# Performance work log

Measured on AMD Instinct MI355X. Metric: run time of the kernel, lower is better.

The kernel has to match this reference:

```python
import jax, jax.numpy as jnp
import numpy as np

DT = 0.001
TAU_MEM = 0.01
TAU_SYN = 0.005
THRESHOLD = 1.0
INITIAL_STATE = 0.0
SS_BETA = 100.0  # SuperSpike surrogate slope (Zenke & Ganguli)


@jax.custom_vjp
def superspike(x):
    # Heaviside spike in forward
    return (x > 0).astype(x.dtype)

def _ss_fwd(x):
    return superspike(x), x

def _ss_bwd(x, g):
    # fast-sigmoid surrogate gradient
    return (g / (SS_BETA * jnp.abs(x) + 1.0) ** 2,)

superspike.defvjp(_ss_fwd, _ss_bwd)


def setup_inputs() -> dict:
    key = jax.random.key(0)
    k1, k2 = jax.random.split(key)
    B, T, IN, OUT = 64, 1024, 256, 256
    inputs = jax.random.normal(k1, (B, T, IN), dtype=jnp.float32)
    w = jax.random.normal(k2, (IN, OUT), dtype=jnp.float32) * 4.0  # scale=4.0 in __init__
    return {"inputs": inputs, "w": w}


def _simulate_mem(inputs, w):
    # inputs: [B, T, IN], w: [IN, OUT]
    x = jnp.matmul(inputs, w)  # [B, T, OUT]
    T = x.shape[1]
    dcy_mem = jnp.exp(jnp.asarray(-DT / (TAU_MEM + 1e-16), dtype=x.dtype))
    scl_mem = 1.0 - dcy_mem
    dcy_syn = jnp.exp(jnp.asarray(-DT / (TAU_SYN + 1e-16), dtype=x.dtype))

    zeros0 = jnp.zeros_like(x[:, 0])  # initial_state = 0

    def step(carry, x_t):
        syn, mem = carry
        new_syn = dcy_syn * syn + x_t
        new_mem = dcy_mem * mem + scl_mem * syn  # uses OLD syn
        out = superspike(mem - THRESHOLD)        # spike from OLD mem
        new_mem = new_mem * (1.0 - out)          # reset
        return (new_syn, new_mem), new_mem

    # loop runs over t = 0 .. T-2 (matches `for t in range(nb_steps - 1)`)
    xs = jnp.swapaxes(x[:, : T - 1], 0, 1)  # [T-1, B, OUT]
    _, mems = jax.lax.scan(step, (zeros0, zeros0), xs)
    mems = jnp.swapaxes(mems, 0, 1)  # [B, T-1, OUT]
    # prepend the initial stored state (zeros, since initial_state=0)
    U = jnp.concatenate([zeros0[:, None, :], mems], axis=1)  # [B, T, OUT]
    return U


def reference(inputs, w):
    # monitor == 'mem' -> return membrane potential trace U
    return _simulate_mem(inputs, w)
```

## Files before the change

kernel.cpp:

```cpp
#include <hip/hip_runtime.h>
#include <cmath>

typedef short bf16x8 __attribute__((ext_vector_type(8)));
typedef float f32x4 __attribute__((ext_vector_type(4)));
typedef unsigned short us4 __attribute__((ext_vector_type(4)));

#define T_DIM 1024
#define LDA 72

__device__ __forceinline__ unsigned short rtn_bf16(float f) {
    unsigned u = __float_as_uint(f);
    return (unsigned short)((u + 0x7FFFu + ((u >> 16) & 1u)) >> 16);
}
__device__ __forceinline__ float bf_to_f(unsigned short h) {
    return __uint_as_float(((unsigned)h) << 16);
}

__global__ __launch_bounds__(256) void lif_wsplit(const float* __restrict__ w,
                                                  unsigned short* __restrict__ wT1,
                                                  unsigned short* __restrict__ wT2,
                                                  unsigned short* __restrict__ wT3) {
    const int id = blockIdx.x * 256 + threadIdx.x;
    const int k = id >> 8, n = id & 255;
    const float f = w[id];
    const unsigned short h1 = rtn_bf16(f);
    const float r1 = f - bf_to_f(h1);
    const unsigned short h2 = rtn_bf16(r1);
    const float r2 = r1 - bf_to_f(h2);
    const unsigned short h3 = rtn_bf16(r2);
    const int o = n * 256 + k;
    wT1[o] = h1; wT2[o] = h2; wT3[o] = h3;
}

__global__ __launch_bounds__(256) void lif_gemm_mfma(const float* __restrict__ in,
                                                     const unsigned short* __restrict__ wT1,
                                                     const unsigned short* __restrict__ wT2,
                                                     const unsigned short* __restrict__ wT3,
                                                     float* __restrict__ xbuf) {
    __shared__ unsigned short As[3][128 * LDA];

    const int tid  = threadIdx.x;
    const int bm   = blockIdx.x;
    const int bn   = blockIdx.y;
    const int wave = tid >> 6;
    const int lane = tid & 63;
    const int l15  = lane & 15;
    const int quad = lane >> 4;
    const int wm   = (wave >> 1) * 64;
    const int wn   = (wave & 1) * 64;

    f32x4 acc[4][4];
    #pragma unroll
    for (int i = 0; i < 4; ++i)
        #pragma unroll
        for (int j = 0; j < 4; ++j) acc[i][j] = (f32x4){0.f, 0.f, 0.f, 0.f};

    const int r  = tid >> 1;
    const int hf = tid & 1;
    const float* arow = in + (size_t)(bm * 128 + r) * 256;

    for (int kt = 0; kt < 4; ++kt) {
        const int k0 = kt * 64;
        float4 av[8];
        #pragma unroll
        for (int j = 0; j < 8; ++j)
            av[j] = *(const float4*)(arow + k0 + (hf * 8 + j) * 4);

        __syncthreads();
        #pragma unroll
        for (int j = 0; j < 8; ++j) {
            const int kl = (hf * 8 + j) * 4;
            float fv[4] = {av[j].x, av[j].y, av[j].z, av[j].w};
            us4 o1, o2, o3;
            #pragma unroll
            for (int i = 0; i < 4; ++i) {
                const unsigned short h1 = rtn_bf16(fv[i]);
                const float r1 = fv[i] - bf_to_f(h1);
                const unsigned short h2 = rtn_bf16(r1);
                const float r2 = r1 - bf_to_f(h2);
                const unsigned short h3 = rtn_bf16(r2);
                o1[i] = h1; o2[i] = h2; o3[i] = h3;
            }
            *(us4*)&As[0][r * LDA + kl] = o1;
            *(us4*)&As[1][r * LDA + kl] = o2;
            *(us4*)&As[2][r * LDA + kl] = o3;
        }
        __syncthreads();

        #pragma unroll
        for (int ks = 0; ks < 2; ++ks) {
            bf16x8 af[3][4];
            #pragma unroll
            for (int mt = 0; mt < 4; ++mt) {
                const int row = wm + mt * 16 + l15;
                const int ko  = ks * 32 + quad * 8;
                af[0][mt] = *(const bf16x8*)&As[0][row * LDA + ko];
                af[1][mt] = *(const bf16x8*)&As[1][row * LDA + ko];
                af[2][mt] = *(const bf16x8*)&As[2][row * LDA + ko];
            }
            #pragma unroll
            for (int nt = 0; nt < 4; ++nt) {
                const int ncol = bn * 128 + wn + nt * 16 + l15;
                const size_t wo = (size_t)ncol * 256 + k0 + ks * 32 + quad * 8;
                const bf16x8 b1 = *(const bf16x8*)(wT1 + wo);
                const bf16x8 b2 = *(const bf16x8*)(wT2 + wo);
                const bf16x8 b3 = *(const bf16x8*)(wT3 + wo);
                #pragma unroll
                for (int mt = 0; mt < 4; ++mt) {
                    f32x4 a = acc[mt][nt];
                    a = __builtin_amdgcn_mfma_f32_16x16x32_bf16(af[0][mt], b1, a, 0, 0, 0);
                    a = __builtin_amdgcn_mfma_f32_16x16x32_bf16(af[0][mt], b2, a, 0, 0, 0);
                    a = __builtin_amdgcn_mfma_f32_16x16x32_bf16(af[1][mt], b1, a, 0, 0, 0);
                    a = __builtin_amdgcn_mfma_f32_16x16x32_bf16(af[1][mt], b2, a, 0, 0, 0);
                    a = __builtin_amdgcn_mfma_f32_16x16x32_bf16(af[0][mt], b3, a, 0, 0, 0);
                    a = __builtin_amdgcn_mfma_f32_16x16x32_bf16(af[2][mt], b1, a, 0, 0, 0);
                    acc[mt][nt] = a;
                }
            }
        }
    }

    #pragma unroll
    for (int mt = 0; mt < 4; ++mt) {
        #pragma unroll
        for (int nt = 0; nt < 4; ++nt) {
            const int C = bn * 128 + wn + nt * 16 + l15;
            const int Rb = bm * 128 + wm + mt * 16 + quad * 4;
            #pragma unroll
            for (int reg = 0; reg < 4; ++reg)
                xbuf[(size_t)(Rb + reg) * 256 + C] = acc[mt][nt][reg];
        }
    }
}

__global__ __launch_bounds__(64) void lif_scan(const float* __restrict__ xbuf,
                                               float* __restrict__ U,
                                               double dcy_syn, double dcy_mem,
                                               double scl_mem) {
    const int b = blockIdx.x >> 2;
    const int o = (blockIdx.x & 3) * 64 + threadIdx.x;

    double syn = 0.0, mem = 0.0;
    U[(size_t)b * T_DIM * 256 + o] = 0.0f;

    const float* xp = xbuf + (size_t)b * T_DIM * 256 + o;
    float* up = U + (size_t)b * T_DIM * 256 + o;

    int tl = 0;
    for (; tl + 32 <= T_DIM - 1; tl += 32) {
        float xr[32];
        #pragma unroll
        for (int j = 0; j < 32; ++j) xr[j] = xp[(size_t)(tl + j) * 256];
        #pragma unroll
        for (int j = 0; j < 32; ++j) {
            double nm = dcy_mem * mem + scl_mem * syn;
            if (mem - 1.0 > 0.0) nm = 0.0;
            syn = dcy_syn * syn + (double)xr[j];
            mem = nm;
            up[(size_t)(tl + j + 1) * 256] = (float)mem;
        }
    }
    for (; tl < T_DIM - 1; ++tl) {
        const double x = (double)xp[(size_t)tl * 256];
        double nm = dcy_mem * mem + scl_mem * syn;
        if (mem - 1.0 > 0.0) nm = 0.0;
        syn = dcy_syn * syn + x;
        mem = nm;
        up[(size_t)(tl + 1) * 256] = (float)mem;
    }
}

extern "C" void kernel_launch(void* const* d_in, const int* in_sizes, int n_in,
                              void* d_out, int out_size, void* d_ws, size_t ws_size,
                              hipStream_t stream) {
    const float* in = (const float*)d_in[0];
    const float* w  = (const float*)d_in[1];
    float* U = (float*)d_out;

    const double dcy_mem = exp(-0.001 / (0.01  + 1e-16));
    const double dcy_syn = exp(-0.001 / (0.005 + 1e-16));
    const double scl_mem = 1.0 - dcy_mem;

    char* ws = (char*)d_ws;
    unsigned short* wT1 = (unsigned short*)ws;
    unsigned short* wT2 = (unsigned short*)(ws + 131072);
    unsigned short* wT3 = (unsigned short*)(ws + 262144);
    float* xbuf = (float*)(ws + 524288);

    lif_wsplit<<<dim3(256), dim3(256), 0, stream>>>(w, wT1, wT2, wT3);
    lif_gemm_mfma<<<dim3(512, 2), dim3(256), 0, stream>>>(in, wT1, wT2, wT3, xbuf);
    lif_scan<<<dim3(256), dim3(64), 0, stream>>>(xbuf, U, dcy_syn, dcy_mem, scl_mem);
}
```

Before: 206.4 us.

## Swizzle GEMM LDS tiles, truncate-split bf16, and stage scan inputs via LDS

The GEMM A-tile now uses an XOR-swizzled 64-wide LDS layout with 8-element vector stores instead of padded rows. The first two bf16 split terms use truncation rather than round-to-nearest. The scan kernel prefetches 64-timestep chunks of x as float4 loads into registers, then into shared memory, double-buffering the next chunk while computing. This targets the scan's strided scalar global loads and LDS bank conflicts, at the cost of extra syncs and register pressure.

```diff
diff --git a/kernel.cpp b/kernel.cpp
--- a/kernel.cpp
+++ b/kernel.cpp
@@ -3,10 +3,9 @@
 
 typedef short bf16x8 __attribute__((ext_vector_type(8)));
 typedef float f32x4 __attribute__((ext_vector_type(4)));
-typedef unsigned short us4 __attribute__((ext_vector_type(4)));
+typedef unsigned short us8v __attribute__((ext_vector_type(8)));
 
 #define T_DIM 1024
-#define LDA 72
 
 __device__ __forceinline__ unsigned short rtn_bf16(float f) {
     unsigned u = __float_as_uint(f);
@@ -14,6 +13,17 @@
 }
 __device__ __forceinline__ float bf_to_f(unsigned short h) {
     return __uint_as_float(((unsigned)h) << 16);
+}
+
+__device__ __forceinline__ void split3(float f, unsigned short& h1,
+                                       unsigned short& h2, unsigned short& h3) {
+    unsigned u = __float_as_uint(f);
+    h1 = (unsigned short)(u >> 16);
+    float r1 = f - __uint_as_float(u & 0xFFFF0000u);
+    unsigned u1 = __float_as_uint(r1);
+    h2 = (unsigned short)(u1 >> 16);
+    float r2 = r1 - __uint_as_float(u1 & 0xFFFF0000u);
+    h3 = rtn_bf16(r2);
 }
 
 __global__ __launch_bounds__(256) void lif_wsplit(const float* __restrict__ w,
@@ -22,12 +32,8 @@
                                                   unsigned short* __restrict__ wT3) {
     const int id = blockIdx.x * 256 + threadIdx.x;
     const int k = id >> 8, n = id & 255;
-    const float f = w[id];
-    const unsigned short h1 = rtn_bf16(f);
-    const float r1 = f - bf_to_f(h1);
-    const unsigned short h2 = rtn_bf16(r1);
-    const float r2 = r1 - bf_to_f(h2);
-    const unsigned short h3 = rtn_bf16(r2);
+    unsigned short h1, h2, h3;
+    split3(w[id], h1, h2, h3);
     const int o = n * 256 + k;
     wT1[o] = h1; wT2[o] = h2; wT3[o] = h3;
 }
@@ -37,7 +43,7 @@
                                                      const unsigned short* __restrict__ wT2,
                                                      const unsigned short* __restrict__ wT3,
                                                      float* __restrict__ xbuf) {
-    __shared__ unsigned short As[3][128 * LDA];
+    __shared__ unsigned short As[3][128 * 64];
 
     const int tid  = threadIdx.x;
     const int bm   = blockIdx.x;
@@ -57,46 +63,45 @@
 
     const int r  = tid >> 1;
     const int hf = tid & 1;
-    const float* arow = in + (size_t)(bm * 128 + r) * 256;
+    const int rx = r & 7;
+    const float* arow = in + (size_t)(bm * 128 + r) * 256 + hf * 32;
 
     for (int kt = 0; kt < 4; ++kt) {
         const int k0 = kt * 64;
         float4 av[8];
         #pragma unroll
         for (int j = 0; j < 8; ++j)
-            av[j] = *(const float4*)(arow + k0 + (hf * 8 + j) * 4);
-
-        __syncthreads();
-        #pragma unroll
-        for (int j = 0; j < 8; ++j) {
-            const int kl = (hf * 8 + j) * 4;
-            float fv[4] = {av[j].x, av[j].y, av[j].z, av[j].w};
-            us4 o1, o2, o3;
-            #pragma unroll
-            for (int i = 0; i < 4; ++i) {
-                const unsigned short h1 = rtn_bf16(fv[i]);
-                const float r1 = fv[i] - bf_to_f(h1);
-                const unsigned short h2 = rtn_bf16(r1);
-                const float r2 = r1 - bf_to_f(h2);
-                const unsigned short h3 = rtn_bf16(r2);
+            av[j] = *(const float4*)(arow + k0 + j * 4);
+
+        __syncthreads();
+        #pragma unroll
+        for (int j2 = 0; j2 < 4; ++j2) {
+            const float fv[8] = {av[2*j2].x, av[2*j2].y, av[2*j2].z, av[2*j2].w,
+                                 av[2*j2+1].x, av[2*j2+1].y, av[2*j2+1].z, av[2*j2+1].w};
+            us8v o1, o2, o3;
+            #pragma unroll
+            for (int i = 0; i < 8; ++i) {
+                unsigned short h1, h2, h3;
+                split3(fv[i], h1, h2, h3);
                 o1[i] = h1; o2[i] = h2; o3[i] = h3;
             }
-            *(us4*)&As[0][r * LDA + kl] = o1;
-            *(us4*)&As[1][r * LDA + kl] = o2;
-            *(us4*)&As[2][r * LDA + kl] = o3;
+            const int cp = ((hf * 4 + j2) ^ rx) * 8;
+            *(us8v*)&As[0][r * 64 + cp] = o1;
+            *(us8v*)&As[1][r * 64 + cp] = o2;
+            *(us8v*)&As[2][r * 64 + cp] = o3;
         }
         __syncthreads();
 
         #pragma unroll
         for (int ks = 0; ks < 2; ++ks) {
             bf16x8 af[3][4];
+            const int ko = ((ks * 4 + quad) ^ (l15 & 7)) * 8;
             #pragma unroll
             for (int mt = 0; mt < 4; ++mt) {
-                const int row = wm + mt * 16 + l15;
-                const int ko  = ks * 32 + quad * 8;
-                af[0][mt] = *(const bf16x8*)&As[0][row * LDA + ko];
-                af[1][mt] = *(const bf16x8*)&As[1][row * LDA + ko];
-                af[2][mt] = *(const bf16x8*)&As[2][row * LDA + ko];
+                const int ro = (wm + mt * 16 + l15) * 64 + ko;
+                af[0][mt] = *(const bf16x8*)&As[0][ro];
+                af[1][mt] = *(const bf16x8*)&As[1][ro];
+                af[2][mt] = *(const bf16x8*)&As[2][ro];
             }
             #pragma unroll
             for (int nt = 0; nt < 4; ++nt) {
@@ -137,36 +142,53 @@
                                                float* __restrict__ U,
                                                double dcy_syn, double dcy_mem,
                                                double scl_mem) {
-    const int b = blockIdx.x >> 2;
-    const int o = (blockIdx.x & 3) * 64 + threadIdx.x;
-
+    __shared__ float xs[64][64];
+
+    const int b    = blockIdx.x >> 2;
+    const int og   = blockIdx.x & 3;
+    const int lane = threadIdx.x;
+
+    const float* src = xbuf + (size_t)b * T_DIM * 256 + og * 64;
+    float* up = U + (size_t)b * T_DIM * 256 + og * 64 + lane;
+
+    up[0] = 0.0f;
     double syn = 0.0, mem = 0.0;
-    U[(size_t)b * T_DIM * 256 + o] = 0.0f;
-
-    const float* xp = xbuf + (size_t)b * T_DIM * 256 + o;
-    float* up = U + (size_t)b * T_DIM * 256 + o;
-
-    int tl = 0;
-    for (; tl + 32 <= T_DIM - 1; tl += 32) {
-        float xr[32];
-        #pragma unroll
-        for (int j = 0; j < 32; ++j) xr[j] = xp[(size_t)(tl + j) * 256];
-        #pragma unroll
-        for (int j = 0; j < 32; ++j) {
+
+    float4 pre[16];
+    #pragma unroll
+    for (int i = 0; i < 16; ++i) {
+        const int f = i * 64 + lane;
+        pre[i] = *(const float4*)(src + (size_t)(f >> 4) * 256 + (f & 15) * 4);
+    }
+
+    for (int c = 0; c < 16; ++c) {
+        __syncthreads();
+        #pragma unroll
+        for (int i = 0; i < 16; ++i) {
+            const int f = i * 64 + lane;
+            *(float4*)&xs[f >> 4][(f & 15) * 4] = pre[i];
+        }
+        __syncthreads();
+        if (c < 15) {
+            const float* nsrc = src + (size_t)(c + 1) * 64 * 256;
+            #pragma unroll
+            for (int i = 0; i < 16; ++i) {
+                const int f = i * 64 + lane;
+                pre[i] = *(const float4*)(nsrc + (size_t)(f >> 4) * 256 + (f & 15) * 4);
+            }
+        }
+        const int tbase = c * 64;
+        #pragma unroll 8
+        for (int j = 0; j < 64; ++j) {
+            const double x = (double)xs[j][lane];
             double nm = dcy_mem * mem + scl_mem * syn;
             if (mem - 1.0 > 0.0) nm = 0.0;
-            syn = dcy_syn * syn + (double)xr[j];
+            syn = dcy_syn * syn + x;
             mem = nm;
-            up[(size_t)(tl + j + 1) * 256] = (float)mem;
-        }
-    }
-    for (; tl < T_DIM - 1; ++tl) {
-        const double x = (double)xp[(size_t)tl * 256];
-        double nm = dcy_mem * mem + scl_mem * syn;
-        if (mem - 1.0 > 0.0) nm = 0.0;
-        syn = dcy_syn * syn + x;
-        mem = nm;
-        up[(size_t)(tl + 1) * 256] = (float)mem;
+            const int t = tbase + j;
+            if (t < T_DIM - 1)
+                up[(size_t)(t + 1) * 256] = (float)mem;
+        }
     }
 }
 
```

Result: slower. 224.4 us (+8.7%).
